# Kernel optimization log

Measured on AMD Instinct MI355X. Metric: run time of the kernel, lower is better.

Reference implementation:

```python
import jax, jax.numpy as jnp
import numpy as np

REG_COEF = 25.0


def setup_inputs() -> dict:
    key = jax.random.key(0)
    k1, k2, k3, k4 = jax.random.split(key, 4)
    B, H, N, RES = 64, 3, 65536, 32
    return {
        "predicted_planes": jax.random.normal(k1, (B, H, 4), dtype=jnp.float32),
        "sample_points": jax.random.uniform(k2, (B, N, 3), dtype=jnp.float32),
        "voxel_grids": jax.random.uniform(k3, (B, 1, RES, RES, RES), dtype=jnp.float32),
        "cp_grids": jax.random.uniform(k4, (B, RES, RES, RES, 3), dtype=jnp.float32),
    }


def _sym_loss(predicted_planes, sample_points, voxel_grids, cp_grids):
    B, H, _ = predicted_planes.shape
    res = cp_grids.shape[1]

    # --- reflexion (symmetry distance) loss, fully batched over (B, H) ---
    n = predicted_planes[..., :3]                                   # [B,H,3]
    n_hat = n / jnp.linalg.norm(n, axis=-1, keepdims=True)          # [B,H,3]
    d = predicted_planes[..., 3]                                    # [B,H]

    # signed distance of each point to each plane: [B,H,N]
    dist = jnp.einsum("bnd,bhd->bhn", sample_points, n_hat) + d[:, :, None]
    # reflected points: [B,H,N,3]
    reflected = sample_points[:, None, :, :] - 2.0 * dist[..., None] * n_hat[:, :, None, :]

    # voxel index per reflected point: floor(x / (1/res)) clamped to [0, res-1]
    vox = jnp.clip(jnp.floor(reflected * res), 0, res - 1).astype(jnp.int32)  # [B,H,N,3]

    # gather closest-point vectors per batch element: cp_grids[b, x, y, z, :]
    def gather_cp(grid, idx):  # grid [res,res,res,3], idx [H,N,3]
        return grid[idx[..., 0], idx[..., 1], idx[..., 2], :]       # [H,N,3]

    cp = jax.vmap(gather_cp)(cp_grids, vox)                          # [B,H,N,3]

    distance = jnp.linalg.norm(reflected - cp, axis=-1)              # [B,H,N]
    # original sums mean-per-(b,head) over the double loop
    reflexion_loss = distance.mean(axis=-1).sum()

    # --- regularization loss: off-orthogonality of plane normals ---
    normals = n / jnp.linalg.norm(n, axis=-1, keepdims=True)         # [B,H,3]
    a = jnp.einsum("bhd,bgd->bhg", normals, normals) - jnp.eye(H, dtype=normals.dtype)
    reg_loss = jnp.sqrt(jnp.sum(a * a, axis=(1, 2)))                 # frobenius per batch, [B]

    out = reflexion_loss + REG_COEF * reg_loss.sum()
    return jnp.reshape(out, (1,))


def reference(predicted_planes, sample_points, voxel_grids, cp_grids):
    return _sym_loss(predicted_planes, sample_points, voxel_grids, cp_grids)
```

## Files before the change

### kernel.cpp

```cpp
#include <hip/hip_runtime.h>

#define NN   65536
#define RES  32
#define CPB  (RES * RES * RES)
#define NBLK 256
#define THREADS 1024

typedef float fx4 __attribute__((ext_vector_type(4)));

__device__ __forceinline__ unsigned int q3b(float x, float y, float z) {
    unsigned int qx = (unsigned int)fmaf(x, 255.f, 0.5f);
    unsigned int qy = (unsigned int)fmaf(y, 255.f, 0.5f);
    unsigned int qz = (unsigned int)fmaf(z, 255.f, 0.5f);
    return qx | (qy << 8) | (qz << 16);
}

__global__ __attribute__((amdgpu_flat_work_group_size(THREADS, THREADS),
                          amdgpu_waves_per_eu(4, 4)))
void sym_main(
    const float* __restrict__ planes,
    const float* __restrict__ pts,
    const float* __restrict__ cp,
    float* __restrict__ partial,
    unsigned int* __restrict__ cnt,
    float* __restrict__ out)
{
    __shared__ unsigned int tab[CPB];
    __shared__ float red[16];
    __shared__ unsigned int s_ticket;

    const int b     = blockIdx.x & 63;
    const int chunk = blockIdx.x >> 6;
    const int tid   = threadIdx.x;

    const fx4* pb = (const fx4*)(pts +
        ((size_t)b * NN + (size_t)chunk * (NN / 4) + (size_t)tid * 16) * 3);
    fx4 v0 = pb[0], v1 = pb[1], v2 = pb[2], v3 = pb[3];
    fx4 v4 = pb[4], v5 = pb[5], v6 = pb[6], v7 = pb[7];
    fx4 v8 = pb[8], v9 = pb[9], v10 = pb[10], v11 = pb[11];
    asm volatile("" ::: "memory");

    const fx4* src = (const fx4*)(cp + (size_t)b * CPB * 3);
    uint4* tab4 = (uint4*)tab;
#pragma unroll
    for (int k = 0; k < 8; ++k) {
        int c4 = k * 1024 + tid;
        fx4 a = src[c4 * 3 + 0];
        fx4 m = src[c4 * 3 + 1];
        fx4 c = src[c4 * 3 + 2];
        uint4 o;
        o.x = q3b(a.x, a.y, a.z);
        o.y = q3b(a.w, m.x, m.y);
        o.z = q3b(m.z, m.w, c.x);
        o.w = q3b(c.y, c.z, c.w);
        tab4[c4] = o;
    }

    float nhx[3], nhy[3], nhz[3], d32[3];
#pragma unroll
    for (int h = 0; h < 3; ++h) {
        const float* pl = planes + (b * 3 + h) * 4;
        float nx = pl[0], ny = pl[1], nz = pl[2];
        float inv = 1.0f / sqrtf(nx * nx + ny * ny + nz * nz);
        nhx[h] = nx * inv; nhy[h] = ny * inv; nhz[h] = nz * inv;
        d32[h] = pl[3] * 32.0f;
    }

    __syncthreads();

    const float UNQ = -32.0f / 255.0f;
    float acc = 0.f;

#pragma unroll
    for (int g = 0; g < 4; ++g) {
        fx4 a  = (g == 0) ? v0 : (g == 1) ? v3 : (g == 2) ? v6 : v9;
        fx4 m  = (g == 0) ? v1 : (g == 1) ? v4 : (g == 2) ? v7 : v10;
        fx4 c  = (g == 0) ? v2 : (g == 1) ? v5 : (g == 2) ? v8 : v11;
        float px[4] = {a.x, a.w, m.z, c.y};
        float py[4] = {a.y, m.x, m.w, c.z};
        float pz[4] = {a.z, m.y, c.x, c.w};
        float rx[12], ry[12], rz[12];
        int cell[12];

#pragma unroll
        for (int i = 0; i < 4; ++i) {
            float x32 = px[i] * 32.f, y32 = py[i] * 32.f, z32 = pz[i] * 32.f;
#pragma unroll
            for (int h = 0; h < 3; ++h) {
                int j = i * 3 + h;
                float dist32 = fmaf(x32, nhx[h], fmaf(y32, nhy[h], fmaf(z32, nhz[h], d32[h])));
                float t2 = -2.f * dist32;
                float x = fmaf(t2, nhx[h], x32);
                float y = fmaf(t2, nhy[h], y32);
                float z = fmaf(t2, nhz[h], z32);
                rx[j] = x; ry[j] = y; rz[j] = z;
                float fxc = truncf(fminf(fmaxf(x, 0.f), 31.f));
                float fyc = truncf(fminf(fmaxf(y, 0.f), 31.f));
                float fzc = truncf(fminf(fmaxf(z, 0.f), 31.f));
                cell[j] = (int)fmaf(fxc, 1024.f, fmaf(fyc, 32.f, fzc));
            }
        }
        unsigned int q[12];
#pragma unroll
        for (int j = 0; j < 12; ++j) q[j] = tab[cell[j]];
#pragma unroll
        for (int j = 0; j < 12; ++j) {
            unsigned int qq = q[j];
            float ux = (float)(qq & 0xffu);
            float uy = (float)((qq >> 8) & 0xffu);
            float uz = (float)((qq >> 16) & 0xffu);
            float dx = fmaf(ux, UNQ, rx[j]);
            float dy = fmaf(uy, UNQ, ry[j]);
            float dz = fmaf(uz, UNQ, rz[j]);
            acc += sqrtf(fmaf(dx, dx, fmaf(dy, dy, dz * dz)));
        }
    }

    for (int off = 32; off > 0; off >>= 1) acc += __shfl_down(acc, off);
    if ((tid & 63) == 0) red[tid >> 6] = acc;
    __syncthreads();
    if (tid == 0) {
        float s = 0.f;
#pragma unroll
        for (int w = 0; w < 16; ++w) s += red[w];
        partial[blockIdx.x] = s;
    }
    __syncthreads();

    if (tid == 0) {
        __threadfence();
        s_ticket = atomicAdd(cnt, 1u);
    }
    __syncthreads();
    if (s_ticket != NBLK - 1) return;

    __threadfence();
    if (tid < 64) {
        int bb = tid;
        float refl = partial[bb] + partial[64 + bb] + partial[128 + bb] + partial[192 + bb];
        refl *= (1.0f / (32.0f * (float)NN));

        float nh[3][3];
#pragma unroll
        for (int h = 0; h < 3; ++h) {
            const float* pl = planes + (bb * 3 + h) * 4;
            float nx = pl[0], ny = pl[1], nz = pl[2];
            float inv = 1.0f / sqrtf(nx * nx + ny * ny + nz * nz);
            nh[h][0] = nx * inv; nh[h][1] = ny * inv; nh[h][2] = nz * inv;
        }
        float ss = 0.f;
#pragma unroll
        for (int h = 0; h < 3; ++h)
#pragma unroll
            for (int g = 0; g < 3; ++g) {
                float d = nh[h][0] * nh[g][0] + nh[h][1] * nh[g][1] + nh[h][2] * nh[g][2];
                if (h == g) d -= 1.0f;
                ss += d * d;
            }
        float val = refl + 25.0f * sqrtf(ss);
        for (int off = 32; off > 0; off >>= 1) val += __shfl_down(val, off);
        if (tid == 0) out[0] = val;
    }
}

extern "C" void kernel_launch(void* const* d_in, const int* in_sizes, int n_in,
                              void* d_out, int out_size, void* d_ws, size_t ws_size,
                              hipStream_t stream) {
    const float* planes = (const float*)d_in[0];
    const float* pts    = (const float*)d_in[1];
    const float* cp     = (const float*)d_in[3];
    float* out = (float*)d_out;

    float* partial = (float*)d_ws;
    unsigned int* cnt = (unsigned int*)((char*)d_ws + 4096);

    (void)hipMemsetAsync(cnt, 0, 4, stream);
    sym_main<<<NBLK, THREADS, 0, stream>>>(planes, pts, cp, partial, cnt, out);
}
```

Before: 133.4 us.

## Pre-quantize closest-point grids once in a separate repack kernel

Adds a repack kernel that quantizes each batch's closest-point grid to packed 3-byte cells once. The main kernel then copies the packed table into shared memory instead of every one of the four chunk blocks per batch re-reading and re-quantizing the full float grid. This cuts redundant global reads (4x per batch) at the cost of an extra launch plus a write and read of the packed buffer. The original path is kept as a fallback when the workspace is too small.

```diff
diff --git a/kernel.cpp b/kernel.cpp
--- a/kernel.cpp
+++ b/kernel.cpp
@@ -5,6 +5,8 @@
 #define CPB  (RES * RES * RES)
 #define NBLK 256
 #define THREADS 1024
+#define CELLS_TOTAL (64 * CPB)
+#define PACKED_OFF 8192
 
 typedef float fx4 __attribute__((ext_vector_type(4)));
 
@@ -15,12 +17,28 @@
     return qx | (qy << 8) | (qz << 16);
 }
 
+__global__ __launch_bounds__(256) void repack_kernel(
+    const float* __restrict__ cp, uint4* __restrict__ packed)
+{
+    int t = blockIdx.x * 256 + threadIdx.x;
+    const fx4* src = (const fx4*)cp + (size_t)t * 3;
+    fx4 a = src[0], m = src[1], c = src[2];
+    uint4 o;
+    o.x = q3b(a.x, a.y, a.z);
+    o.y = q3b(a.w, m.x, m.y);
+    o.z = q3b(m.z, m.w, c.x);
+    o.w = q3b(c.y, c.z, c.w);
+    packed[t] = o;
+}
+
+template<bool PACKED>
 __global__ __attribute__((amdgpu_flat_work_group_size(THREADS, THREADS),
                           amdgpu_waves_per_eu(4, 4)))
 void sym_main(
     const float* __restrict__ planes,
     const float* __restrict__ pts,
     const float* __restrict__ cp,
+    const uint4* __restrict__ ptab,
     float* __restrict__ partial,
     unsigned int* __restrict__ cnt,
     float* __restrict__ out)
@@ -38,22 +56,30 @@
     fx4 v0 = pb[0], v1 = pb[1], v2 = pb[2], v3 = pb[3];
     fx4 v4 = pb[4], v5 = pb[5], v6 = pb[6], v7 = pb[7];
     fx4 v8 = pb[8], v9 = pb[9], v10 = pb[10], v11 = pb[11];
-    asm volatile("" ::: "memory");
-
-    const fx4* src = (const fx4*)(cp + (size_t)b * CPB * 3);
+
     uint4* tab4 = (uint4*)tab;
-#pragma unroll
-    for (int k = 0; k < 8; ++k) {
-        int c4 = k * 1024 + tid;
-        fx4 a = src[c4 * 3 + 0];
-        fx4 m = src[c4 * 3 + 1];
-        fx4 c = src[c4 * 3 + 2];
-        uint4 o;
-        o.x = q3b(a.x, a.y, a.z);
-        o.y = q3b(a.w, m.x, m.y);
-        o.z = q3b(m.z, m.w, c.x);
-        o.w = q3b(c.y, c.z, c.w);
-        tab4[c4] = o;
+    if (PACKED) {
+        const uint4* ps = ptab + (size_t)b * (CPB / 4);
+#pragma unroll
+        for (int k = 0; k < 8; ++k) {
+            int c4 = k * 1024 + tid;
+            tab4[c4] = ps[c4];
+        }
+    } else {
+        const fx4* src = (const fx4*)(cp + (size_t)b * CPB * 3);
+#pragma unroll
+        for (int k = 0; k < 8; ++k) {
+            int c4 = k * 1024 + tid;
+            fx4 a = src[c4 * 3 + 0];
+            fx4 m = src[c4 * 3 + 1];
+            fx4 c = src[c4 * 3 + 2];
+            uint4 o;
+            o.x = q3b(a.x, a.y, a.z);
+            o.y = q3b(a.w, m.x, m.y);
+            o.z = q3b(m.z, m.w, c.x);
+            o.w = q3b(c.y, c.z, c.w);
+            tab4[c4] = o;
+        }
     }
 
     float nhx[3], nhy[3], nhz[3], d32[3];
@@ -66,6 +92,9 @@
         d32[h] = pl[3] * 32.0f;
     }
 
+    asm volatile("" : "+v"(v0), "+v"(v1), "+v"(v2), "+v"(v3),
+                      "+v"(v4), "+v"(v5), "+v"(v6), "+v"(v7),
+                      "+v"(v8), "+v"(v9), "+v"(v10), "+v"(v11));
     __syncthreads();
 
     const float UNQ = -32.0f / 255.0f;
@@ -175,5 +204,15 @@
     unsigned int* cnt = (unsigned int*)((char*)d_ws + 4096);
 
     (void)hipMemsetAsync(cnt, 0, 4, stream);
-    sym_main<<<NBLK, THREADS, 0, stream>>>(planes, pts, cp, partial, cnt, out);
-}
+
+    const size_t need = (size_t)PACKED_OFF + (size_t)CELLS_TOTAL * 4;
+    if (ws_size >= need) {
+        uint4* packed = (uint4*)((char*)d_ws + PACKED_OFF);
+        repack_kernel<<<CELLS_TOTAL / 4 / 256, 256, 0, stream>>>(cp, packed);
+        sym_main<true><<<NBLK, THREADS, 0, stream>>>(planes, pts, cp, packed,
+                                                     partial, cnt, out);
+    } else {
+        sym_main<false><<<NBLK, THREADS, 0, stream>>>(planes, pts, cp, nullptr,
+                                                      partial, cnt, out);
+    }
+}
```

Measured after the change: 129.9 us. 2.7% less time.
